# Kernel tuning notes

Hardware: AMD Instinct MI355X
Metric: run time of the kernel (lower is better)

## Reference

```python
import jax, jax.numpy as jnp
import numpy as np

N, E, F_IN, HID, EDIM = 20000, 320000, 16, 64, 1


def _add_self_loops(src, dst, eattr, n):
    # PyG add_self_loops with fill_value='mean': self-loop edge_attr = mean of
    # incoming edge_attr per destination node (0 if no incoming edges).
    deg = jax.ops.segment_sum(jnp.ones_like(eattr[:, 0]), dst, num_segments=n)
    mean_attr = jax.ops.segment_sum(eattr, dst, num_segments=n) / jnp.maximum(deg, 1.0)[:, None]
    loop = jnp.arange(n)
    return (jnp.concatenate([src, loop]), jnp.concatenate([dst, loop]),
            jnp.concatenate([eattr, mean_attr], axis=0))


def _gat_layer(x, src, dst, eattr, W, a_src, a_dst, We, a_e, b, heads, out_ch, n):
    # shared linear for src/dst (PyG GATConv with int in_channels)
    h = (x @ W).reshape(n, heads, out_ch)                      # [N,H,C]
    al_s = jnp.einsum('nhc,hc->nh', h, a_src)                  # [N,H]
    al_d = jnp.einsum('nhc,hc->nh', h, a_dst)
    ef = (eattr @ We).reshape(-1, heads, out_ch)               # [E,H,C]
    al_e = jnp.einsum('ehc,hc->eh', ef, a_e)                   # [E,H]
    alpha = jax.nn.leaky_relu(al_s[src] + al_d[dst] + al_e, 0.2)
    # segment softmax over destination node
    m = jax.ops.segment_max(alpha, dst, num_segments=n)
    m = jnp.where(jnp.isfinite(m), m, 0.0)
    ex = jnp.exp(alpha - m[dst])
    den = jax.ops.segment_sum(ex, dst, num_segments=n)
    coef = ex / (den[dst] + 1e-16)                             # [E,H]
    out = jax.ops.segment_sum(h[src] * coef[:, :, None], dst, num_segments=n)
    return out.reshape(n, heads * out_ch) + b


def setup_inputs() -> dict:
    key = jax.random.key(0)
    ks = jax.random.split(key, 24)
    s = 0.1
    inp = {
        'x': jax.random.normal(ks[0], (N, F_IN), jnp.float32),
        'edge_index': jax.random.randint(ks[1], (2, E), 0, N, jnp.int64),
        'edge_attr': jax.random.uniform(ks[2], (E, EDIM), jnp.float32),
        # layer 0: heads=4, in=16, out=64
        'W0': jax.random.normal(ks[3], (F_IN, 4 * HID), jnp.float32) * s,
        'as0': jax.random.normal(ks[4], (4, HID), jnp.float32) * s,
        'ad0': jax.random.normal(ks[5], (4, HID), jnp.float32) * s,
        'We0': jax.random.normal(ks[6], (EDIM, 4 * HID), jnp.float32) * s,
        'ae0': jax.random.normal(ks[7], (4, HID), jnp.float32) * s,
        'b0': jnp.zeros((4 * HID,), jnp.float32),
        # layer 1: heads=4, in=256, out=64
        'W1': jax.random.normal(ks[8], (4 * HID, 4 * HID), jnp.float32) * s,
        'as1': jax.random.normal(ks[9], (4, HID), jnp.float32) * s,
        'ad1': jax.random.normal(ks[10], (4, HID), jnp.float32) * s,
        'We1': jax.random.normal(ks[11], (EDIM, 4 * HID), jnp.float32) * s,
        'ae1': jax.random.normal(ks[12], (4, HID), jnp.float32) * s,
        'b1': jnp.zeros((4 * HID,), jnp.float32),
        # layer 2: heads=1, in=256, out=64
        'W2': jax.random.normal(ks[13], (4 * HID, HID), jnp.float32) * s,
        'as2': jax.random.normal(ks[14], (1, HID), jnp.float32) * s,
        'ad2': jax.random.normal(ks[15], (1, HID), jnp.float32) * s,
        'We2': jax.random.normal(ks[16], (EDIM, HID), jnp.float32) * s,
        'ae2': jax.random.normal(ks[17], (1, HID), jnp.float32) * s,
        'b2': jnp.zeros((HID,), jnp.float32),
        'ln_g': jnp.ones((HID,), jnp.float32),
        'ln_b': jnp.zeros((HID,), jnp.float32),
    }
    return inp


def reference(x, edge_index, edge_attr,
              W0, as0, ad0, We0, ae0, b0,
              W1, as1, ad1, We1, ae1, b1,
              W2, as2, ad2, We2, ae2, b2,
              ln_g, ln_b):
    n = x.shape[0]
    src, dst, eattr = _add_self_loops(edge_index[0], edge_index[1], edge_attr, n)
    h = _gat_layer(x, src, dst, eattr, W0, as0, ad0, We0, ae0, b0, 4, HID, n)
    h = jax.nn.elu(h)  # dropout is identity in eval
    h = _gat_layer(h, src, dst, eattr, W1, as1, ad1, We1, ae1, b1, 4, HID, n)
    h = jax.nn.elu(h)
    h = _gat_layer(h, src, dst, eattr, W2, as2, ad2, We2, ae2, b2, 1, HID, n)
    mu = jnp.mean(h, axis=-1, keepdims=True)
    var = jnp.mean((h - mu) ** 2, axis=-1, keepdims=True)
    return (h - mu) / jnp.sqrt(var + 1e-5) * ln_g + ln_b
```

## Files before the change

kernel.cpp:

```cpp
#include <hip/hip_runtime.h>
#include <hip/hip_bf16.h>
#include <math.h>


typedef __attribute__((ext_vector_type(8))) short short8;
typedef __attribute__((ext_vector_type(4))) float float4v;

#define CAP 64

__device__ __forceinline__ float wave_sum(float v) {
#pragma unroll
  for (int off = 32; off > 0; off >>= 1) v += __shfl_xor(v, off, 64);
  return v;
}

__device__ __forceinline__ unsigned short f2bf(float v) {
  unsigned u = __float_as_uint(v);
  unsigned r = u + 0x7fff + ((u >> 16) & 1);
  return (unsigned short)(r >> 16);
}

__device__ __forceinline__ float bf2f(unsigned short u) {
  return __uint_as_float(((unsigned)u) << 16);
}

__device__ __forceinline__ float sel4(float a, float b, float c, float d, int i) {
  return (i == 0) ? a : (i == 1) ? b : (i == 2) ? c : d;
}

__global__ __launch_bounds__(256) void k1_kernel(
    const float* __restrict__ x, const int* __restrict__ srcv, const int* __restrict__ dstv,
    const float* __restrict__ eattr,
    const float* __restrict__ W0, const float* __restrict__ as0, const float* __restrict__ ad0,
    const float* __restrict__ We0, const float* __restrict__ ae0,
    const float* __restrict__ W1, const float* __restrict__ as1, const float* __restrict__ ad1,
    const float* __restrict__ We1, const float* __restrict__ ae1,
    const float* __restrict__ W2, const float* __restrict__ as2, const float* __restrict__ ad2,
    const float* __restrict__ We2, const float* __restrict__ ae2,
    unsigned short* __restrict__ Wf1, unsigned short* __restrict__ Wf2,
    float* __restrict__ wedot, float* __restrict__ al0s, float* __restrict__ al0d,
    int* __restrict__ deg, int2* __restrict__ ebuf,
    int N, int E, int gD) {
  int b = blockIdx.x;
  int tid = threadIdx.x;
  if (b < 272) {
    int idx = b * 256 + tid;
    int j = idx & 7, lane = (idx >> 3) & 63, ks = (idx >> 9) & 7, nt = idx >> 12;
    int k = ks * 32 + (lane >> 4) * 8 + j;
    int col = lane & 15;
    float v = 0.f;
    if (nt < 16) {
      v = W1[(size_t)k * 256 + nt * 16 + col];
    } else if (col < 4) {
      for (int c = 0; c < 64; c++) v = fmaf(W1[(size_t)k * 256 + col * 64 + c], as1[col * 64 + c], v);
    } else if (col < 8) {
      int h = col - 4;
      for (int c = 0; c < 64; c++) v = fmaf(W1[(size_t)k * 256 + h * 64 + c], ad1[h * 64 + c], v);
    }
    Wf1[idx] = f2bf(v);
  } else if (b < 352) {
    int idx = (b - 272) * 256 + tid;
    int j = idx & 7, lane = (idx >> 3) & 63, ks = (idx >> 9) & 7, nt = idx >> 12;
    int k = ks * 32 + (lane >> 4) * 8 + j;
    int col = lane & 15;
    float v = 0.f;
    if (nt < 4) {
      v = W2[(size_t)k * 64 + nt * 16 + col];
    } else if (col < 1) {
      for (int c = 0; c < 64; c++) v = fmaf(W2[(size_t)k * 64 + c], as2[c], v);
    } else if (col < 2) {
      for (int c = 0; c < 64; c++) v = fmaf(W2[(size_t)k * 64 + c], ad2[c], v);
    }
    Wf2[idx] = f2bf(v);
  } else if (b == 352) {
    if (tid >= 64) return;
    int c = tid;
    for (int h = 0; h < 4; h++) {
      float v = wave_sum(We0[h * 64 + c] * ae0[h * 64 + c]);
      if (c == 0) wedot[h] = v;
    }
    for (int h = 0; h < 4; h++) {
      float v = wave_sum(We1[h * 64 + c] * ae1[h * 64 + c]);
      if (c == 0) wedot[4 + h] = v;
    }
    float v = wave_sum(We2[c] * ae2[c]);
    if (c == 0) wedot[8] = v;
  } else if (b < 353 + gD) {
    __shared__ float va[128];
    if (tid < 128) {
      int k = tid >> 3, col = tid & 7;
      float v = 0.f;
      if (col < 4) {
        for (int c = 0; c < 64; c++) v = fmaf(W0[(size_t)k * 256 + col * 64 + c], as0[col * 64 + c], v);
      } else {
        int h = col - 4;
        for (int c = 0; c < 64; c++) v = fmaf(W0[(size_t)k * 256 + h * 64 + c], ad0[h * 64 + c], v);
      }
      va[tid] = v;
    }
    __syncthreads();
    int node = (b - 353) * 256 + tid;
    if (node >= N) return;
    const float4* xr = (const float4*)(x + (size_t)node * 16);
    float4 xv[4];
#pragma unroll
    for (int q = 0; q < 4; q++) xv[q] = xr[q];
    float al[8];
#pragma unroll
    for (int j = 0; j < 8; j++) al[j] = 0.f;
#pragma unroll
    for (int k = 0; k < 16; k++) {
      float xk = ((const float*)xv)[k];
#pragma unroll
      for (int j = 0; j < 8; j++) al[j] = fmaf(xk, va[k * 8 + j], al[j]);
    }
    ((float4*)al0s)[node] = make_float4(al[0], al[1], al[2], al[3]);
    ((float4*)al0d)[node] = make_float4(al[4], al[5], al[6], al[7]);
  } else {
    int e = (b - 353 - gD) * 256 + tid;
    if (e >= E) return;
    int d = dstv[e];
    int s = srcv[e];
    float ea = eattr[e];
    int pos = atomicAdd(&deg[d], 1);
    if (pos < CAP) ebuf[(size_t)d * CAP + pos] = make_int2(s, __float_as_int(ea));
  }
}

__global__ __launch_bounds__(256) void fused0_kernel(
    const int* __restrict__ deg, const int2* __restrict__ ebuf,
    const float* __restrict__ al0s, const float* __restrict__ al0d,
    const float* __restrict__ wedot,
    const float* __restrict__ x, const float* __restrict__ W0,
    const float* __restrict__ b0, const unsigned short* __restrict__ Wf1,
    unsigned short* __restrict__ buf256, float* __restrict__ al1s,
    float* __restrict__ al1d, int n) {
  __shared__ unsigned short hrow[16][264];
  __shared__ __align__(16) float wbuf[4][16][4];
  __shared__ int sbuf[4][16];
  int tile = blockIdx.x;
  int wv = threadIdx.x >> 6;
  int lane = threadIdx.x & 63;
  int es = lane >> 4;
  int c = lane & 15;
  int le = lane >> 2;
  int lh = lane & 3;

  for (int s = 0; s < 4; s++) {
    int r = wv * 4 + s;
    int node = tile * 16 + r;
    if (node < n) {
      int dg = deg[node];
      int cnt = dg < CAP ? dg : CAP;
      float xself = x[(size_t)node * 16 + c];
      float4 as4s = ((const float4*)al0s)[node];
      float4 ald4 = ((const float4*)al0d)[node];
      float aldP = ((const float*)&ald4)[0];
      aldP = sel4(ald4.x, ald4.y, ald4.z, ald4.w, lh);
      float wd0 = wedot[0], wd1 = wedot[1], wd2 = wedot[2], wd3 = wedot[3];
      float wdP = sel4(wd0, wd1, wd2, wd3, lh);

      float Z[4] = {0.f, 0.f, 0.f, 0.f};
      float denP = 0.f;
      float easumP = 0.f;

      for (int i = 0; i < cnt; i += 16) {
        int slot = i + le;
        bool av = slot < cnt;
        int2 re = ebuf[(size_t)node * CAP + slot];
        int srcE = av ? re.x : 0;
        float ev = av ? __int_as_float(re.y) : 0.f;
        float a = al0s[(size_t)srcE * 4 + lh] + aldP + ev * wdP;
        a = fmaxf(a, 0.2f * a);
        a = fminf(a, 30.f);
        float wE = av ? __expf(a) : 0.f;
        denP += wE;
        easumP += (lh == 0) ? ev : 0.f;
        wbuf[wv][le][lh] = wE;
        if (lh == 0) sbuf[wv][le] = srcE;
#pragma unroll
        for (int k = 0; k < 4; k++) {
          int e = k * 4 + es;
          float4 w4 = *(const float4*)&wbuf[wv][e][0];
          int srcX = sbuf[wv][e];
          float xv = x[(size_t)srcX * 16 + c];
          Z[0] = fmaf(w4.x, xv, Z[0]);
          Z[1] = fmaf(w4.y, xv, Z[1]);
          Z[2] = fmaf(w4.z, xv, Z[2]);
          Z[3] = fmaf(w4.w, xv, Z[3]);
        }
      }

#pragma unroll
      for (int h = 0; h < 4; h++) {
        Z[h] += __shfl_xor(Z[h], 16, 64);
        Z[h] += __shfl_xor(Z[h], 32, 64);
      }
      denP += __shfl_xor(denP, 4, 64);
      denP += __shfl_xor(denP, 8, 64);
      denP += __shfl_xor(denP, 16, 64);
      denP += __shfl_xor(denP, 32, 64);
      float easum = wave_sum(easumP);

      float dsel = __shfl(denP, es, 64);
      float evs = easum / fmaxf((float)dg, 1.f);
      float as_e = sel4(as4s.x, as4s.y, as4s.z, as4s.w, es);
      float ald_e = sel4(ald4.x, ald4.y, ald4.z, ald4.w, es);
      float wd_e = sel4(wd0, wd1, wd2, wd3, es);
      float aS = as_e + ald_e + evs * wd_e;
      aS = fmaxf(aS, 0.2f * aS);
      aS = fminf(aS, 30.f);
      float wvs = __expf(aS);
      dsel += wvs;
      float zsel = sel4(Z[0], Z[1], Z[2], Z[3], es) + wvs * xself;
      float zn = zsel / (dsel + 1e-16f);

      float4 w0r[16];
#pragma unroll
      for (int cc = 0; cc < 16; cc++) w0r[cc] = ((const float4*)(W0 + (size_t)cc * 256))[lane];
      float zc[16];
      int basel = lane & 48;
#pragma unroll
      for (int cc = 0; cc < 16; cc++) zc[cc] = __shfl(zn, basel + cc, 64);
      float o[4];
      float4 b4 = ((const float4*)b0)[lane];
#pragma unroll
      for (int jj = 0; jj < 4; jj++) o[jj] = ((const float*)&b4)[jj];
#pragma unroll
      for (int cc = 0; cc < 16; cc++) {
#pragma unroll
        for (int jj = 0; jj < 4; jj++) o[jj] = fmaf(zc[cc], ((const float*)&w0r[cc])[jj], o[jj]);
      }
      ushort4 o4;
      float ox = o[0] > 0.f ? o[0] : expm1f(o[0]);
      float oy = o[1] > 0.f ? o[1] : expm1f(o[1]);
      float oz = o[2] > 0.f ? o[2] : expm1f(o[2]);
      float ow = o[3] > 0.f ? o[3] : expm1f(o[3]);
      o4.x = f2bf(ox);
      o4.y = f2bf(oy);
      o4.z = f2bf(oz);
      o4.w = f2bf(ow);
      *(ushort4*)&hrow[r][lane * 4] = o4;
    } else {
      *(ushort4*)&hrow[r][lane * 4] = make_ushort4(0, 0, 0, 0);
    }
  }
  __syncthreads();

  int m = lane & 15, q = lane >> 4;
  int row0 = tile * 16;
  short8 afrag[8];
#pragma unroll
  for (int ks = 0; ks < 8; ks++) afrag[ks] = *(short8*)&hrow[m][ks * 32 + q * 8];

  const short8* wf = (const short8*)Wf1;
  for (int nt = wv; nt < 17; nt += 4) {
    const short8* bl = wf + (size_t)nt * 8 * 64 + lane;
    short8 bf[8];
#pragma unroll
    for (int ks = 0; ks < 8; ks++) bf[ks] = bl[ks * 64];
    float4v acc = {0.f, 0.f, 0.f, 0.f};
#pragma unroll
    for (int ks = 0; ks < 8; ks++)
      acc = __builtin_amdgcn_mfma_f32_16x16x32_bf16(afrag[ks], bf[ks], acc, 0, 0, 0);
    if (nt < 16) {
      int col = nt * 16 + m;
#pragma unroll
      for (int reg = 0; reg < 4; reg++) {
        int rr = row0 + q * 4 + reg;
        if (rr < n) buf256[(size_t)rr * 256 + col] = f2bf(acc[reg]);
      }
    } else {
#pragma unroll
      for (int reg = 0; reg < 4; reg++) {
        int rr = row0 + q * 4 + reg;
        if (rr < n) {
          if (m < 4) al1s[(size_t)rr * 4 + m] = acc[reg];
          else if (m < 8) al1d[(size_t)rr * 4 + (m - 4)] = acc[reg];
        }
      }
    }
  }
}

__global__ __launch_bounds__(256) void fused1_kernel(
    const int* __restrict__ deg, const int2* __restrict__ ebuf,
    const float* __restrict__ al1s, const float* __restrict__ al1d,
    const float* __restrict__ wedot,
    const unsigned short* __restrict__ buf256, const float* __restrict__ b1,
    const unsigned short* __restrict__ Wf2, unsigned short* __restrict__ buf64,
    float* __restrict__ al2s, float* __restrict__ al2d, int n) {
  __shared__ unsigned short hrow[16][264];
  __shared__ __align__(16) float wbuf[4][16][4];
  __shared__ int sbuf[4][16];
  int tile = blockIdx.x;
  int wv = threadIdx.x >> 6;
  int lane = threadIdx.x & 63;
  int half = lane >> 5;
  int l = lane & 31;
  int h4 = l >> 3;
  int le = lane >> 2;
  int lh = lane & 3;

  for (int s = 0; s < 4; s++) {
    int r = wv * 4 + s;
    int node = tile * 16 + r;
    if (node < n) {
      int dg = deg[node];
      int cnt = dg < CAP ? dg : CAP;
      float aldh = al1d[(size_t)node * 4 + h4];
      float alsh = al1s[(size_t)node * 4 + h4];
      float wdh = wedot[4 + h4];
      float aldP = al1d[(size_t)node * 4 + lh];
      float wdP = wedot[4 + lh];
      short8 rowS = ((const short8*)(buf256 + (size_t)node * 256))[l];

      float acc[8];
#pragma unroll
      for (int j = 0; j < 8; j++) acc[j] = 0.f;
      float denP = 0.f;
      float easumP = 0.f;

      for (int i = 0; i < cnt; i += 16) {
        int slot = i + le;
        bool av = slot < cnt;
        int2 re = ebuf[(size_t)node * CAP + slot];
        int srcE = av ? re.x : 0;
        float ev = av ? __int_as_float(re.y) : 0.f;
        float a = al1s[(size_t)srcE * 4 + lh] + aldP + ev * wdP;
        a = fmaxf(a, 0.2f * a);
        a = fminf(a, 30.f);
        float wE = av ? __expf(a) : 0.f;
        denP += wE;
        easumP += (lh == 0) ? ev : 0.f;
        wbuf[wv][le][lh] = wE;
        if (lh == 0) sbuf[wv][le] = srcE;
#pragma unroll
        for (int k = 0; k < 4; k++) {
          int eA = k * 4 + (half ? 1 : 0);
          int eB = k * 4 + (half ? 3 : 2);
          float wA = wbuf[wv][eA][h4];
          float wB = wbuf[wv][eB][h4];
          int srcA = sbuf[wv][eA];
          int srcB = sbuf[wv][eB];
          short8 rowA = ((const short8*)(buf256 + (size_t)srcA * 256))[l];
          short8 rowB = ((const short8*)(buf256 + (size_t)srcB * 256))[l];
          const unsigned short* pa = (const unsigned short*)&rowA;
          const unsigned short* pb = (const unsigned short*)&rowB;
#pragma unroll
          for (int j = 0; j < 8; j++) acc[j] = fmaf(wA, bf2f(pa[j]), acc[j]);
#pragma unroll
          for (int j = 0; j < 8; j++) acc[j] = fmaf(wB, bf2f(pb[j]), acc[j]);
        }
      }

#pragma unroll
      for (int j = 0; j < 8; j++) acc[j] += __shfl_xor(acc[j], 32, 64);
      denP += __shfl_xor(denP, 4, 64);
      denP += __shfl_xor(denP, 8, 64);
      denP += __shfl_xor(denP, 16, 64);
      denP += __shfl_xor(denP, 32, 64);
      float easum = wave_sum(easumP);
      float den = __shfl(denP, h4, 64);

      {
        float evs = easum / fmaxf((float)dg, 1.f);
        float a = alsh + aldh + evs * wdh;
        a = fmaxf(a, 0.2f * a);
        a = fminf(a, 30.f);
        float wvv = __expf(a);
        const unsigned short* ps = (const unsigned short*)&rowS;
        den += wvv;
#pragma unroll
        for (int j = 0; j < 8; j++) acc[j] = fmaf(wvv, bf2f(ps[j]), acc[j]);
      }

      if (half == 0) {
        float inv = 1.f / (den + 1e-16f);
        float4 bb0 = ((const float4*)b1)[l * 2];
        float4 bb1 = ((const float4*)b1)[l * 2 + 1];
        unsigned short o8[8];
#pragma unroll
        for (int j = 0; j < 8; j++) {
          float bjv = (j < 4) ? ((const float*)&bb0)[j] : ((const float*)&bb1)[j - 4];
          float o = acc[j] * inv + bjv;
          o = o > 0.f ? o : expm1f(o);
          o8[j] = f2bf(o);
        }
        *(short8*)&hrow[r][l * 8] = *(short8*)o8;
      }
    } else if ((lane >> 5) == 0) {
      unsigned short z8[8] = {0, 0, 0, 0, 0, 0, 0, 0};
      *(short8*)&hrow[r][(lane & 31) * 8] = *(short8*)z8;
    }
  }
  __syncthreads();

  int m = lane & 15, q = lane >> 4;
  int row0 = tile * 16;
  short8 afrag[8];
#pragma unroll
  for (int ks = 0; ks < 8; ks++) afrag[ks] = *(short8*)&hrow[m][ks * 32 + q * 8];

  const short8* wf = (const short8*)Wf2;
  for (int nt = wv; nt < 5; nt += 4) {
    const short8* bl = wf + (size_t)nt * 8 * 64 + lane;
    short8 bf[8];
#pragma unroll
    for (int ks = 0; ks < 8; ks++) bf[ks] = bl[ks * 64];
    float4v acc = {0.f, 0.f, 0.f, 0.f};
#pragma unroll
    for (int ks = 0; ks < 8; ks++)
      acc = __builtin_amdgcn_mfma_f32_16x16x32_bf16(afrag[ks], bf[ks], acc, 0, 0, 0);
    if (nt < 4) {
      int col = nt * 16 + m;
#pragma unroll
      for (int reg = 0; reg < 4; reg++) {
        int rr = row0 + q * 4 + reg;
        if (rr < n) buf64[(size_t)rr * 64 + col] = f2bf(acc[reg]);
      }
    } else {
#pragma unroll
      for (int reg = 0; reg < 4; reg++) {
        int rr = row0 + q * 4 + reg;
        if (rr < n) {
          if (m < 1) al2s[rr] = acc[reg];
          else if (m < 2) al2d[rr] = acc[reg];
        }
      }
    }
  }
}

__global__ __launch_bounds__(256) void agg_ln_kernel(
    const int* __restrict__ deg, const int2* __restrict__ ebuf,
    const float* __restrict__ al2s, const float* __restrict__ al2d,
    const float* __restrict__ wedot,
    const unsigned short* __restrict__ B, const float* __restrict__ bias,
    const float* __restrict__ ln_g, const float* __restrict__ ln_b,
    float* __restrict__ out, int n) {
  __shared__ float wbuf[4][16];
  __shared__ int sbuf[4][16];
  int wv = threadIdx.x >> 6;
  int node = blockIdx.x * 4 + wv;
  if (node >= n) return;
  int lane = threadIdx.x & 63;
  int q = lane >> 4;
  int l = lane & 15;
  int le = lane & 15;
  int dg = deg[node];
  int cnt = dg < CAP ? dg : CAP;
  float ald = al2d[node];
  float als = al2s[node];
  float wd = wedot[0];
  ushort4 bvS = ((const ushort4*)(B + (size_t)node * 64))[l];

  float4 acc = make_float4(0.f, 0.f, 0.f, 0.f);
  float denP = 0.f;
  float easumP = 0.f;

  for (int i = 0; i < cnt; i += 16) {
    int slot = i + le;
    bool av = slot < cnt;
    int2 re = ebuf[(size_t)node * CAP + slot];
    int srcE = av ? re.x : 0;
    float ev = av ? __int_as_float(re.y) : 0.f;
    float a = al2s[srcE] + ald + ev * wd;
    a = fmaxf(a, 0.2f * a);
    a = fminf(a, 30.f);
    float wE = av ? __expf(a) : 0.f;
    denP += wE;
    easumP += ev;
    if (lane < 16) {
      wbuf[wv][le] = wE;
      sbuf[wv][le] = srcE;
    }
#pragma unroll
    for (int k = 0; k < 4; k++) {
      int e = k * 4 + q;
      float w = wbuf[wv][e];
      int src = sbuf[wv][e];
      ushort4 bv = ((const ushort4*)(B + (size_t)src * 64))[l];
      acc.x = fmaf(w, bf2f(bv.x), acc.x);
      acc.y = fmaf(w, bf2f(bv.y), acc.y);
      acc.z = fmaf(w, bf2f(bv.z), acc.z);
      acc.w = fmaf(w, bf2f(bv.w), acc.w);
    }
  }

  acc.x += __shfl_xor(acc.x, 32, 64);
  acc.y += __shfl_xor(acc.y, 32, 64);
  acc.z += __shfl_xor(acc.z, 32, 64);
  acc.w += __shfl_xor(acc.w, 32, 64);
  acc.x += __shfl_xor(acc.x, 16, 64);
  acc.y += __shfl_xor(acc.y, 16, 64);
  acc.z += __shfl_xor(acc.z, 16, 64);
  acc.w += __shfl_xor(acc.w, 16, 64);
  float den = wave_sum(denP) * 0.25f;
  float easum = wave_sum(easumP) * 0.25f;

  {
    float evs = easum / fmaxf((float)dg, 1.f);
    float a = als + ald + evs * wd;
    a = fmaxf(a, 0.2f * a);
    a = fminf(a, 30.f);
    float wv2 = __expf(a);
    den += wv2;
    acc.x = fmaf(wv2, bf2f(bvS.x), acc.x);
    acc.y = fmaf(wv2, bf2f(bvS.y), acc.y);
    acc.z = fmaf(wv2, bf2f(bvS.z), acc.z);
    acc.w = fmaf(wv2, bf2f(bvS.w), acc.w);
  }

  float inv = 1.f / (den + 1e-16f);
  float4 b4 = ((const float4*)bias)[l];
  float4 o;
  o.x = acc.x * inv + b4.x;
  o.y = acc.y * inv + b4.y;
  o.z = acc.z * inv + b4.z;
  o.w = acc.w * inv + b4.w;
  float s = (o.x + o.y) + (o.z + o.w);
#pragma unroll
  for (int off = 1; off < 16; off <<= 1) s += __shfl_xor(s, off, 64);
  float mu = s * (1.f / 64.f);
  float dx = o.x - mu, dy = o.y - mu, dz = o.z - mu, dw = o.w - mu;
  float v = (dx * dx + dy * dy) + (dz * dz + dw * dw);
#pragma unroll
  for (int off = 1; off < 16; off <<= 1) v += __shfl_xor(v, off, 64);
  float rs = rsqrtf(v * (1.f / 64.f) + 1e-5f);
  if (q == 0) {
    float4 g4 = ((const float4*)ln_g)[l];
    float4 lb4 = ((const float4*)ln_b)[l];
    float4 rr;
    rr.x = dx * rs * g4.x + lb4.x;
    rr.y = dy * rs * g4.y + lb4.y;
    rr.z = dz * rs * g4.z + lb4.z;
    rr.w = dw * rs * g4.w + lb4.w;
    ((float4*)(out + (size_t)node * 64))[l] = rr;
  }
}

extern "C" void kernel_launch(void* const* d_in, const int* in_sizes, int n_in,
                              void* d_out, int out_size, void* d_ws, size_t ws_size,
                              hipStream_t stream) {
  const float* x = (const float*)d_in[0];
  const int* ei = (const int*)d_in[1];
  const float* eattr = (const float*)d_in[2];
  const float* W0 = (const float*)d_in[3];
  const float* as0 = (const float*)d_in[4];
  const float* ad0 = (const float*)d_in[5];
  const float* We0 = (const float*)d_in[6];
  const float* ae0 = (const float*)d_in[7];
  const float* b0 = (const float*)d_in[8];
  const float* W1 = (const float*)d_in[9];
  const float* as1 = (const float*)d_in[10];
  const float* ad1 = (const float*)d_in[11];
  const float* We1 = (const float*)d_in[12];
  const float* ae1 = (const float*)d_in[13];
  const float* b1 = (const float*)d_in[14];
  const float* W2 = (const float*)d_in[15];
  const float* as2 = (const float*)d_in[16];
  const float* ad2 = (const float*)d_in[17];
  const float* We2 = (const float*)d_in[18];
  const float* ae2 = (const float*)d_in[19];
  const float* b2 = (const float*)d_in[20];
  const float* lng = (const float*)d_in[21];
  const float* lnb = (const float*)d_in[22];
  float* outp = (float*)d_out;

  const int N = in_sizes[0] / 16;
  const int E = in_sizes[1] / 2;
  const int* srcv = ei;
  const int* dstv = ei + E;

  char* w = (char*)d_ws;
  size_t off = 0;
  auto alloc = [&](size_t bytes) -> void* {
    void* p = w + off;
    off += (bytes + 255) & ~(size_t)255;
    return p;
  };
  int* deg = (int*)alloc((size_t)N * 4);
  size_t zero_bytes = off;
  int2* ebuf = (int2*)alloc(((size_t)N * CAP + 16) * 8);
  float* wedot = (float*)alloc(16 * 4);
  float* al0s = (float*)alloc((size_t)N * 4 * 4);
  float* al0d = (float*)alloc((size_t)N * 4 * 4);
  float* al1s = (float*)alloc((size_t)N * 4 * 4);
  float* al1d = (float*)alloc((size_t)N * 4 * 4);
  float* al2s = (float*)alloc((size_t)N * 4);
  float* al2d = (float*)alloc((size_t)N * 4);
  unsigned short* Wf1 = (unsigned short*)alloc((size_t)17 * 4096 * 2);
  unsigned short* Wf2 = (unsigned short*)alloc((size_t)5 * 4096 * 2);
  unsigned short* buf256 = (unsigned short*)alloc((size_t)N * 256 * 2);
  unsigned short* buf64 = (unsigned short*)alloc((size_t)N * 64 * 2);
  (void)ws_size;

  hipMemsetAsync(d_ws, 0, zero_bytes, stream);

  int gE = (E + 255) / 256;
  int gD = (N + 255) / 256;

  k1_kernel<<<353 + gD + gE, 256, 0, stream>>>(
      x, srcv, dstv, eattr, W0, as0, ad0, We0, ae0, W1, as1, ad1, We1, ae1,
      W2, as2, ad2, We2, ae2, Wf1, Wf2, wedot, al0s, al0d, deg, ebuf, N, E, gD);

  int gT = (N + 15) / 16;
  int gNode4 = (N + 3) / 4;

  fused0_kernel<<<gT, 256, 0, stream>>>(deg, ebuf, al0s, al0d, wedot, x, W0, b0,
                                        Wf1, buf256, al1s, al1d, N);

  fused1_kernel<<<gT, 256, 0, stream>>>(deg, ebuf, al1s, al1d, wedot, buf256, b1,
                                        Wf2, buf64, al2s, al2d, N);

  agg_ln_kernel<<<gNode4, 256, 0, stream>>>(deg, ebuf, al2s, al2d, wedot + 8,
                                            buf64, b2, lng, lnb, outp, N);
}
```

Baseline: 215.7 us.

## Replace LDS edge staging with shuffles and prefetch gathered rows before softmax

In all three aggregation kernels, per-edge source indices and weights are now exchanged with wave shuffles instead of being written to and read back from shared memory. The gathered neighbour rows (x, buf256, B) are issued right after the edge record is read, before the exp and softmax arithmetic, so their latency can overlap that math. In the first kernel W0 is also staged once per block into LDS instead of being held as 16 float4 registers per lane. The changes add register pressure from the prefetched rows and use 16 KB of LDS in fused0, which may reduce occupancy.

```diff
diff --git a/kernel.cpp b/kernel.cpp
--- a/kernel.cpp
+++ b/kernel.cpp
@@ -136,8 +136,7 @@
     unsigned short* __restrict__ buf256, float* __restrict__ al1s,
     float* __restrict__ al1d, int n) {
   __shared__ unsigned short hrow[16][264];
-  __shared__ __align__(16) float wbuf[4][16][4];
-  __shared__ int sbuf[4][16];
+  __shared__ float w0lds[4096];
   int tile = blockIdx.x;
   int wv = threadIdx.x >> 6;
   int lane = threadIdx.x & 63;
@@ -145,6 +144,13 @@
   int c = lane & 15;
   int le = lane >> 2;
   int lh = lane & 3;
+
+#pragma unroll
+  for (int i = 0; i < 4; i++) {
+    int idx = i * 256 + threadIdx.x;
+    ((float4*)w0lds)[idx] = ((const float4*)W0)[idx];
+  }
+  __syncthreads();
 
   for (int s = 0; s < 4; s++) {
     int r = wv * 4 + s;
@@ -155,8 +161,7 @@
       float xself = x[(size_t)node * 16 + c];
       float4 as4s = ((const float4*)al0s)[node];
       float4 ald4 = ((const float4*)al0d)[node];
-      float aldP = ((const float*)&ald4)[0];
-      aldP = sel4(ald4.x, ald4.y, ald4.z, ald4.w, lh);
+      float aldP = sel4(ald4.x, ald4.y, ald4.z, ald4.w, lh);
       float wd0 = wedot[0], wd1 = wedot[1], wd2 = wedot[2], wd3 = wedot[3];
       float wdP = sel4(wd0, wd1, wd2, wd3, lh);
 
@@ -170,24 +175,29 @@
         int2 re = ebuf[(size_t)node * CAP + slot];
         int srcE = av ? re.x : 0;
         float ev = av ? __int_as_float(re.y) : 0.f;
+        int srcK[4];
+        float xvK[4];
+#pragma unroll
+        for (int k = 0; k < 4; k++) srcK[k] = __shfl(srcE, (k * 4 + es) * 4, 64);
+#pragma unroll
+        for (int k = 0; k < 4; k++) xvK[k] = x[(size_t)srcK[k] * 16 + c];
         float a = al0s[(size_t)srcE * 4 + lh] + aldP + ev * wdP;
         a = fmaxf(a, 0.2f * a);
         a = fminf(a, 30.f);
         float wE = av ? __expf(a) : 0.f;
         denP += wE;
         easumP += (lh == 0) ? ev : 0.f;
-        wbuf[wv][le][lh] = wE;
-        if (lh == 0) sbuf[wv][le] = srcE;
 #pragma unroll
         for (int k = 0; k < 4; k++) {
-          int e = k * 4 + es;
-          float4 w4 = *(const float4*)&wbuf[wv][e][0];
-          int srcX = sbuf[wv][e];
-          float xv = x[(size_t)srcX * 16 + c];
-          Z[0] = fmaf(w4.x, xv, Z[0]);
-          Z[1] = fmaf(w4.y, xv, Z[1]);
-          Z[2] = fmaf(w4.z, xv, Z[2]);
-          Z[3] = fmaf(w4.w, xv, Z[3]);
+          int e4 = (k * 4 + es) * 4;
+          float w0v = __shfl(wE, e4 + 0, 64);
+          float w1v = __shfl(wE, e4 + 1, 64);
+          float w2v = __shfl(wE, e4 + 2, 64);
+          float w3v = __shfl(wE, e4 + 3, 64);
+          Z[0] = fmaf(w0v, xvK[k], Z[0]);
+          Z[1] = fmaf(w1v, xvK[k], Z[1]);
+          Z[2] = fmaf(w2v, xvK[k], Z[2]);
+          Z[3] = fmaf(w3v, xvK[k], Z[3]);
         }
       }
 
@@ -215,9 +225,6 @@
       float zsel = sel4(Z[0], Z[1], Z[2], Z[3], es) + wvs * xself;
       float zn = zsel / (dsel + 1e-16f);
 
-      float4 w0r[16];
-#pragma unroll
-      for (int cc = 0; cc < 16; cc++) w0r[cc] = ((const float4*)(W0 + (size_t)cc * 256))[lane];
       float zc[16];
       int basel = lane & 48;
 #pragma unroll
@@ -228,8 +235,9 @@
       for (int jj = 0; jj < 4; jj++) o[jj] = ((const float*)&b4)[jj];
 #pragma unroll
       for (int cc = 0; cc < 16; cc++) {
-#pragma unroll
-        for (int jj = 0; jj < 4; jj++) o[jj] = fmaf(zc[cc], ((const float*)&w0r[cc])[jj], o[jj]);
+        float4 w0r = *(const float4*)&w0lds[cc * 256 + lane * 4];
+#pragma unroll
+        for (int jj = 0; jj < 4; jj++) o[jj] = fmaf(zc[cc], ((const float*)&w0r)[jj], o[jj]);
       }
       ushort4 o4;
       float ox = o[0] > 0.f ? o[0] : expm1f(o[0]);
@@ -291,8 +299,6 @@
     const unsigned short* __restrict__ Wf2, unsigned short* __restrict__ buf64,
     float* __restrict__ al2s, float* __restrict__ al2d, int n) {
   __shared__ unsigned short hrow[16][264];
-  __shared__ __align__(16) float wbuf[4][16][4];
-  __shared__ int sbuf[4][16];
   int tile = blockIdx.x;
   int wv = threadIdx.x >> 6;
   int lane = threadIdx.x & 63;
@@ -301,6 +307,8 @@
   int h4 = l >> 3;
   int le = lane >> 2;
   int lh = lane & 3;
+  int eA0 = half ? 1 : 0;
+  int eB0 = half ? 3 : 2;
 
   for (int s = 0; s < 4; s++) {
     int r = wv * 4 + s;
@@ -327,26 +335,30 @@
         int2 re = ebuf[(size_t)node * CAP + slot];
         int srcE = av ? re.x : 0;
         float ev = av ? __int_as_float(re.y) : 0.f;
+        int srcA[4], srcB[4];
+#pragma unroll
+        for (int k = 0; k < 4; k++) {
+          srcA[k] = __shfl(srcE, (k * 4 + eA0) * 4, 64);
+          srcB[k] = __shfl(srcE, (k * 4 + eB0) * 4, 64);
+        }
+        short8 rowA[4], rowB[4];
+#pragma unroll
+        for (int k = 0; k < 4; k++) {
+          rowA[k] = ((const short8*)(buf256 + (size_t)srcA[k] * 256))[l];
+          rowB[k] = ((const short8*)(buf256 + (size_t)srcB[k] * 256))[l];
+        }
         float a = al1s[(size_t)srcE * 4 + lh] + aldP + ev * wdP;
         a = fmaxf(a, 0.2f * a);
         a = fminf(a, 30.f);
         float wE = av ? __expf(a) : 0.f;
         denP += wE;
         easumP += (lh == 0) ? ev : 0.f;
-        wbuf[wv][le][lh] = wE;
-        if (lh == 0) sbuf[wv][le] = srcE;
 #pragma unroll
         for (int k = 0; k < 4; k++) {
-          int eA = k * 4 + (half ? 1 : 0);
-          int eB = k * 4 + (half ? 3 : 2);
-          float wA = wbuf[wv][eA][h4];
-          float wB = wbuf[wv][eB][h4];
-          int srcA = sbuf[wv][eA];
-          int srcB = sbuf[wv][eB];
-          short8 rowA = ((const short8*)(buf256 + (size_t)srcA * 256))[l];
-          short8 rowB = ((const short8*)(buf256 + (size_t)srcB * 256))[l];
-          const unsigned short* pa = (const unsigned short*)&rowA;
-          const unsigned short* pb = (const unsigned short*)&rowB;
+          float wA = __shfl(wE, (k * 4 + eA0) * 4 + h4, 64);
+          float wB = __shfl(wE, (k * 4 + eB0) * 4 + h4, 64);
+          const unsigned short* pa = (const unsigned short*)&rowA[k];
+          const unsigned short* pb = (const unsigned short*)&rowB[k];
 #pragma unroll
           for (int j = 0; j < 8; j++) acc[j] = fmaf(wA, bf2f(pa[j]), acc[j]);
 #pragma unroll
@@ -439,8 +451,6 @@
     const unsigned short* __restrict__ B, const float* __restrict__ bias,
     const float* __restrict__ ln_g, const float* __restrict__ ln_b,
     float* __restrict__ out, int n) {
-  __shared__ float wbuf[4][16];
-  __shared__ int sbuf[4][16];
   int wv = threadIdx.x >> 6;
   int node = blockIdx.x * 4 + wv;
   if (node >= n) return;
@@ -465,26 +475,25 @@
     int2 re = ebuf[(size_t)node * CAP + slot];
     int srcE = av ? re.x : 0;
     float ev = av ? __int_as_float(re.y) : 0.f;
+    int srcK[4];
+#pragma unroll
+    for (int k = 0; k < 4; k++) srcK[k] = __shfl(srcE, k * 4 + q, 64);
+    ushort4 bvK[4];
+#pragma unroll
+    for (int k = 0; k < 4; k++) bvK[k] = ((const ushort4*)(B + (size_t)srcK[k] * 64))[l];
     float a = al2s[srcE] + ald + ev * wd;
     a = fmaxf(a, 0.2f * a);
     a = fminf(a, 30.f);
     float wE = av ? __expf(a) : 0.f;
     denP += wE;
     easumP += ev;
-    if (lane < 16) {
-      wbuf[wv][le] = wE;
-      sbuf[wv][le] = srcE;
-    }
 #pragma unroll
     for (int k = 0; k < 4; k++) {
-      int e = k * 4 + q;
-      float w = wbuf[wv][e];
-      int src = sbuf[wv][e];
-      ushort4 bv = ((const ushort4*)(B + (size_t)src * 64))[l];
-      acc.x = fmaf(w, bf2f(bv.x), acc.x);
-      acc.y = fmaf(w, bf2f(bv.y), acc.y);
-      acc.z = fmaf(w, bf2f(bv.z), acc.z);
-      acc.w = fmaf(w, bf2f(bv.w), acc.w);
+      float w = __shfl(wE, k * 4 + q, 64);
+      acc.x = fmaf(w, bf2f(bvK[k].x), acc.x);
+      acc.y = fmaf(w, bf2f(bvK[k].y), acc.y);
+      acc.z = fmaf(w, bf2f(bvK[k].z), acc.z);
+      acc.w = fmaf(w, bf2f(bvK[k].w), acc.w);
     }
   }
 
```

New measurement: 210.6 us. 2.4% less time.
